# Kernel optimization log

Hardware: AMD Instinct MI355X
Metric: run time of the kernel (lower is better)

## Reference

```python
import jax, jax.numpy as jnp
import numpy as np

V, E, U, D, B, T = 32000, 256, 512, 512, 32, 64


def setup_inputs() -> dict:
    key = jax.random.key(0)
    ks = jax.random.split(key, 12)
    g = lambda k, shape: (jax.random.normal(k, shape, jnp.float32) * 0.05)
    return dict(
        x=jax.random.randint(ks[0], (B, T), 0, V),
        emb=g(ks[1], (V, E)),
        Wxf=g(ks[2], (E, 4 * U)), Whf=g(ks[3], (U, 4 * U)), bf=jnp.zeros((4 * U,), jnp.float32),
        Wxb=g(ks[4], (E, 4 * U)), Whb=g(ks[5], (U, 4 * U)), bb=jnp.zeros((4 * U,), jnp.float32),
        W1=g(ks[6], (2 * U + D, 10)), b1=jnp.zeros((10,), jnp.float32),
        W2=g(ks[7], (10, 1)), b2=jnp.zeros((1,), jnp.float32),
        Wxd=g(ks[8], (2 * U, 4 * D)), Whd=g(ks[9], (D, 4 * D)), bd=jnp.zeros((4 * D,), jnp.float32),
        Wo=g(ks[10], (D, V)), bo=jnp.zeros((V,), jnp.float32),
    )


def lstm_cell(x_t, h, c, Wx, Wh, b):
    # Keras gate order: i, f, g(cell), o
    z = x_t @ Wx + h @ Wh + b
    i, f, g, o = jnp.split(z, 4, axis=-1)
    c = jax.nn.sigmoid(f) * c + jax.nn.sigmoid(i) * jnp.tanh(g)
    h = jax.nn.sigmoid(o) * jnp.tanh(c)
    return h, c


def lstm_seq(xs, Wx, Wh, b):
    # xs: [T, B, F] -> hidden states [T, B, units]
    units = Wh.shape[0]
    h0 = jnp.zeros((xs.shape[1], units), xs.dtype)

    def step(carry, x_t):
        h, c = lstm_cell(x_t, carry[0], carry[1], Wx, Wh, b)
        return (h, c), h

    _, hs = jax.lax.scan(step, (h0, h0), xs)
    return hs


def reference(x, emb, Wxf, Whf, bf, Wxb, Whb, bb, W1, b1, W2, b2, Wxd, Whd, bd, Wo, bo):
    Bsz, Tlen = x.shape
    xe = emb[x]                              # [B, T, E]
    xs = jnp.swapaxes(xe, 0, 1)              # [T, B, E]
    hf = lstm_seq(xs, Wxf, Whf, bf)          # forward direction
    hb = lstm_seq(xs[::-1], Wxb, Whb, bb)[::-1]  # backward direction
    a = jnp.swapaxes(jnp.concatenate([hf, hb], axis=-1), 0, 1)  # [B, T, 2U]
    du = Whd.shape[0]

    def dec_step(carry, _):
        h, c = carry
        s_rep = jnp.broadcast_to(h[:, None, :], (Bsz, Tlen, du))
        cat = jnp.concatenate([a, s_rep], axis=-1)              # [B, T, 2U+D]
        e = jax.nn.relu(jnp.tanh(cat @ W1 + b1) @ W2 + b2)      # [B, T, 1]
        score = jax.nn.softmax(e, axis=1)
        ctx = jnp.sum(score * a, axis=1)                        # [B, 2U]
        h, c = lstm_cell(ctx, h, c, Wxd, Whd, bd)
        out = jax.nn.softmax(h @ Wo + bo, axis=-1)              # [B, V]
        return (h, c), out

    init = (jnp.zeros((Bsz, du), a.dtype), jnp.zeros((Bsz, du), a.dtype))
    _, outs = jax.lax.scan(dec_step, init, None, length=Tlen)
    return jnp.swapaxes(outs, 0, 1)  # [B, T, V]
```

## Files before the change

### kernel.cpp

```cpp
#include <hip/hip_runtime.h>
#include <hip/hip_bf16.h>
#include <cstdint>

typedef float f32x4 __attribute__((ext_vector_type(4)));
typedef __bf16 bf16x8 __attribute__((ext_vector_type(8)));

__device__ __forceinline__ uint32_t bf1(float x) {
  uint32_t u = __float_as_uint(x);
  return (u + 0x7fffu + ((u >> 16) & 1u)) >> 16;
}
__device__ __forceinline__ uint32_t bpack(float lo, float hi) {
  return bf1(lo) | (bf1(hi) << 16);
}
__device__ __forceinline__ float blo(uint32_t u) { return __uint_as_float(u << 16); }
__device__ __forceinline__ float bhi(uint32_t u) { return __uint_as_float(u & 0xffff0000u); }
__device__ __forceinline__ float sigm(float x) {
  return __fdividef(1.f, 1.f + exp2f(x * -1.4426950408889634f));
}
__device__ __forceinline__ float tanhf_fast(float x) {
  float e2 = exp2f(x * 2.8853900817779268f);
  return 1.f - __fdividef(2.f, e2 + 1.f);
}

__device__ __forceinline__ float dot2bf(uint32_t a, uint32_t b, float acc) {
  asm("v_dot2_f32_bf16 %0, %1, %2, %0" : "+v"(acc) : "v"(a), "v"(b));
  return acc;
}

#define GLOAD_LDS16(g, l)                                                     \
  __builtin_amdgcn_global_load_lds(                                           \
      (const __attribute__((address_space(1))) void*)(g),                     \
      (__attribute__((address_space(3))) void*)(l), 16, 0, 0)

__global__ __launch_bounds__(256) void k0_pack(
    const float* __restrict__ Whf, const float* __restrict__ Whb,
    uint32_t* __restrict__ Wencp, const float* __restrict__ Whd,
    uint32_t* __restrict__ Wdp, const float* __restrict__ W1,
    uint32_t* __restrict__ W1pbAll)
{
  int bid = blockIdx.x;
  if (bid < 4096) {
    int p = bid * 256 + threadIdx.x;
    int e = p & 3, c = (p >> 2) & 7, k4p = (p >> 5) & 63;
    int blk = (p >> 11) & 255, dir = p >> 19;
    int k2 = 4 * k4p + e;
    const float* W = dir ? Whb : Whf;
    int col = (c >> 1) * 512 + blk * 2 + (c & 1);
    Wencp[p] = bpack(W[(size_t)(2 * k2) * 2048 + col],
                     W[(size_t)(2 * k2 + 1) * 2048 + col]);
  } else if (bid < 6144) {
    int p = (bid - 4096) * 256 + threadIdx.x;
    int e = p & 3, cc = (p >> 2) & 31, q4 = (p >> 7) & 63, ug = p >> 13;
    int k2 = 4 * q4 + e;
    int col = (cc >> 3) * 512 + ug * 8 + (cc & 7);
    int k = 2 * k2;
    Wdp[p] = bpack(Whd[(size_t)k * 2048 + col], Whd[(size_t)(k + 1) * 2048 + col]);
  } else {
    int p = (bid - 6144) * 256 + threadIdx.x;
    if (p < 9216) {
      int q = p / 12, j = p % 12;
      float v0 = (j < 10) ? W1[(size_t)(2 * q) * 10 + j] : 0.f;
      float v1 = (j < 10) ? W1[(size_t)(2 * q + 1) * 10 + j] : 0.f;
      W1pbAll[p] = bpack(v0, v1);
    }
  }
}

__global__ __launch_bounds__(256) void k1_embed_gemm(
    const int* __restrict__ x, const float* __restrict__ emb,
    const float* __restrict__ Wxf, const float* __restrict__ Wxb,
    const float* __restrict__ bfv, const float* __restrict__ bbv,
    float* __restrict__ Xf, float* __restrict__ Xb)
{
  __shared__ float As[32 * 260];
  __shared__ float Bs[32 * 128];
  __shared__ int xid[32];
  const int t = threadIdx.x;
  const int ty = blockIdx.y;
  const int c0 = blockIdx.x * 128;
  if (t < 32) xid[t] = x[t * 64 + ty];
  __syncthreads();
  for (int i = 0; i < 8; ++i) {
    int f4 = t + 256 * i;
    int r = f4 >> 6, k4 = (f4 & 63) << 2;
    float4 v = *(const float4*)(emb + (size_t)xid[r] * 256 + k4);
    *(float4*)(&As[r * 260 + k4]) = v;
  }
  const int isB = (c0 >= 2048);
  const float* Wsrc = isB ? Wxb : Wxf;
  const float* bias = isB ? bbv : bfv;
  const int cbase = c0 & 2047;
  float acc[4][4] = {};
  const int rq = t >> 5;
  const int cq = t & 31;
  for (int kc = 0; kc < 8; ++kc) {
    int k0 = kc * 32;
    __syncthreads();
    for (int i = 0; i < 4; ++i) {
      int f4 = t + 256 * i;
      int k = f4 >> 5, c4 = (f4 & 31) << 2;
      *(float4*)(&Bs[k * 128 + c4]) =
          *(const float4*)(Wsrc + (size_t)(k0 + k) * 2048 + cbase + c4);
    }
    __syncthreads();
#pragma unroll
    for (int kk = 0; kk < 32; ++kk) {
      float a0 = As[(4 * rq + 0) * 260 + k0 + kk];
      float a1 = As[(4 * rq + 1) * 260 + k0 + kk];
      float a2 = As[(4 * rq + 2) * 260 + k0 + kk];
      float a3 = As[(4 * rq + 3) * 260 + k0 + kk];
      float4 b = *(const float4*)(&Bs[kk * 128 + 4 * cq]);
      acc[0][0] += a0 * b.x; acc[0][1] += a0 * b.y; acc[0][2] += a0 * b.z; acc[0][3] += a0 * b.w;
      acc[1][0] += a1 * b.x; acc[1][1] += a1 * b.y; acc[1][2] += a1 * b.z; acc[1][3] += a1 * b.w;
      acc[2][0] += a2 * b.x; acc[2][1] += a2 * b.y; acc[2][2] += a2 * b.z; acc[2][3] += a2 * b.w;
      acc[3][0] += a3 * b.x; acc[3][1] += a3 * b.y; acc[3][2] += a3 * b.z; acc[3][3] += a3 * b.w;
    }
  }
  float* Xout = isB ? Xb : Xf;
  for (int i = 0; i < 4; ++i) {
    int c = cbase + 4 * cq + i;
    float bi = bias[c];
    for (int j = 0; j < 4; ++j) {
      int b_ = 4 * rq + j;
      Xout[((size_t)ty * 2048 + c) * 32 + b_] = acc[j][i] + bi;
    }
  }
}

__global__ __launch_bounds__(256) void k2_enc_step(
    const float* __restrict__ Xf, const float* __restrict__ Xb,
    const uint32_t* __restrict__ Wencp,
    const uint32_t* __restrict__ hfi, uint32_t* __restrict__ hfo,
    const uint32_t* __restrict__ hbi, uint32_t* __restrict__ hbo,
    float* __restrict__ cf, float* __restrict__ cb,
    ushort* __restrict__ aB, int step)
{
  __shared__ uint32_t hTp[256 * 32];
  __shared__ uint32_t Wsp[2048];
  __shared__ float zx[8 * 33];
  __shared__ float zbuf[32 * 9];
  __shared__ float hl[2 * 32];
  const int t = threadIdx.x;
  const int dir = blockIdx.x >> 8;
  const int blk = blockIdx.x & 255;
  const int u0 = blk * 2;
  const float* XF = dir ? Xb : Xf;
  const uint32_t* hin = dir ? hbi : hfi;
  uint32_t* hout = dir ? hbo : hfo;
  float* cst = dir ? cb : cf;
  const int ta = dir ? (63 - step) : step;
  const uint32_t* wsrc = Wencp + ((size_t)dir * 256 + blk) * 2048;

  for (int i = 0; i < 8; ++i) {
    int b4 = (t >> 6) * 64 + 256 * i;
    GLOAD_LDS16(hin + (size_t)(t + 256 * i) * 4, hTp + (size_t)b4 * 4);
  }
  for (int i = 0; i < 2; ++i) {
    int b4 = (t >> 6) * 64 + 256 * i;
    GLOAD_LDS16(wsrc + (size_t)(t + 256 * i) * 4, Wsp + (size_t)b4 * 4);
  }
  {
    int c = t >> 5, r = t & 31;
    int col = (c >> 1) * 512 + u0 + (c & 1);
    zx[c * 33 + r] = XF[((size_t)ta * 2048 + col) * 32 + r];
  }
  __syncthreads();
  const int r = t & 31, cc = t >> 5;
  float acc = zx[cc * 33 + r];
  const uint4* hT4 = (const uint4*)hTp;
  const uint4* Ws4 = (const uint4*)Wsp;
#pragma unroll 8
  for (int k4p = 0; k4p < 64; ++k4p) {
    uint4 ua = hT4[k4p * 32 + r];
    uint4 w = Ws4[k4p * 8 + cc];
    acc = dot2bf(ua.x, w.x, acc);
    acc = dot2bf(ua.y, w.y, acc);
    acc = dot2bf(ua.z, w.z, acc);
    acc = dot2bf(ua.w, w.w, acc);
  }
  zbuf[r * 9 + cc] = acc;
  __syncthreads();
  if (t < 64) {
    int rr = t & 31, j = t >> 5;
    float zi = zbuf[rr * 9 + j];
    float zf = zbuf[rr * 9 + 2 + j];
    float zg = zbuf[rr * 9 + 4 + j];
    float zo = zbuf[rr * 9 + 6 + j];
    int u = u0 + j;
    float cold = cst[u * 32 + rr];
    float cn = sigm(zf) * cold + sigm(zi) * tanhf_fast(zg);
    float h = sigm(zo) * tanhf_fast(cn);
    cst[u * 32 + rr] = cn;
    aB[((size_t)rr * 64 + ta) * 1024 + dir * 512 + u] = (ushort)bf1(h);
    hl[j * 32 + rr] = h;
  }
  __syncthreads();
  if (t < 32) {
    hout[(blk >> 2) * 128 + t * 4 + (blk & 3)] = bpack(hl[t], hl[32 + t]);
  }
}

__global__ __launch_bounds__(256) void k5_aw1(
    const ushort* __restrict__ aB, const uint32_t* __restrict__ W1pbAll,
    const float* __restrict__ b1, float* __restrict__ aw1)
{
  __shared__ uint32_t ar[512];
  __shared__ float ps[16 * 17];
  const int t = threadIdx.x;
  const uint32_t* aBu = (const uint32_t*)aB;
  for (int m = blockIdx.x; m < 2048; m += gridDim.x) {
    __syncthreads();
    *(uint2*)(&ar[t * 2]) = *(const uint2*)(aBu + (size_t)m * 512 + t * 2);
    __syncthreads();
    int j = t & 15, part = t >> 4;
    int jj = j < 10 ? j : 0;
    float s = 0.f;
#pragma unroll 8
    for (int q = part * 32; q < part * 32 + 32; ++q)
      s = dot2bf(ar[q], W1pbAll[q * 12 + jj], s);
    ps[part * 17 + j] = s;
    __syncthreads();
    if (t < 16) {
      float sum = 0.f;
      if (t < 10) {
        for (int p = 0; p < 16; ++p) sum += ps[p * 17 + t];
        sum += b1[t];
      }
      aw1[m * 16 + t] = sum;
    }
  }
}

__global__ __launch_bounds__(256) void k_wxdT(
    const float* __restrict__ Wxd, ushort* __restrict__ WxdT)
{
  __shared__ float tile[64 * 65];
  const int t = threadIdx.x;
  const int n0 = blockIdx.x * 64, k0 = blockIdx.y * 64;
  for (int i = 0; i < 16; ++i) {
    int p = t + 256 * i;
    int kk = p >> 6, nn = p & 63;
    tile[kk * 65 + nn] = Wxd[(size_t)(k0 + kk) * 2048 + n0 + nn];
  }
  __syncthreads();
  for (int i = 0; i < 4; ++i) {
    int p = t + 256 * i;
    int nn = p >> 4, k4 = (p & 15) * 4;
    ushort4 o;
    o.x = (ushort)bf1(tile[(k4 + 0) * 65 + nn]);
    o.y = (ushort)bf1(tile[(k4 + 1) * 65 + nn]);
    o.z = (ushort)bf1(tile[(k4 + 2) * 65 + nn]);
    o.w = (ushort)bf1(tile[(k4 + 3) * 65 + nn]);
    *(ushort4*)(WxdT + (size_t)(n0 + nn) * 1024 + k0 + k4) = o;
  }
}

__global__ __launch_bounds__(256) void kA_aprime(
    const ushort* __restrict__ WxdT, const ushort* __restrict__ aB,
    uint32_t* __restrict__ ApTb)
{
  __shared__ ushort As[128 * 64];
  __shared__ ushort Bs[128 * 64];
  const int t = threadIdx.x;
  const int lane = t & 63, w = t >> 6;
  const int wr = w >> 1, wc = w & 1;
  const int m0 = blockIdx.y * 128, n0 = blockIdx.x * 128;
  const int lrow = lane >> 3, s = lane & 7;
  const int quad = lane >> 4, l15 = lane & 15;
  f32x4 acc[4][4] = {};
  for (int kc = 0; kc < 16; ++kc) {
    const int k0 = kc * 64;
    __syncthreads();
    for (int i = 0; i < 4; ++i) {
      int row = w * 32 + i * 8 + lrow;
      int k8 = s ^ (row & 7);
      GLOAD_LDS16(WxdT + (size_t)(m0 + row) * 1024 + k0 + k8 * 8,
                  As + (w * 32 + i * 8) * 64);
      GLOAD_LDS16(aB + (size_t)(n0 + row) * 1024 + k0 + k8 * 8,
                  Bs + (w * 32 + i * 8) * 64);
    }
    __syncthreads();
#pragma unroll
    for (int ks = 0; ks < 2; ++ks) {
      bf16x8 af[4], bfr[4];
      int kq = ks * 4 + quad;
#pragma unroll
      for (int mi = 0; mi < 4; ++mi) {
        int row = wr * 64 + mi * 16 + l15;
        int slot = kq ^ (row & 7);
        af[mi] = *(const bf16x8*)(As + row * 64 + slot * 8);
      }
#pragma unroll
      for (int ni = 0; ni < 4; ++ni) {
        int row = wc * 64 + ni * 16 + l15;
        int slot = kq ^ (row & 7);
        bfr[ni] = *(const bf16x8*)(Bs + row * 64 + slot * 8);
      }
#pragma unroll
      for (int mi = 0; mi < 4; ++mi)
#pragma unroll
        for (int ni = 0; ni < 4; ++ni)
          acc[mi][ni] = __builtin_amdgcn_mfma_f32_16x16x32_bf16(
              af[mi], bfr[ni], acc[mi][ni], 0, 0, 0);
    }
  }
#pragma unroll
  for (int mi = 0; mi < 4; ++mi) {
    int mbase = m0 + wr * 64 + mi * 16 + quad * 4;
#pragma unroll
    for (int reg = 0; reg < 4; ++reg) {
      int m = mbase + reg;
#pragma unroll
      for (int ni = 0; ni < 4; ++ni) {
        int n = n0 + wc * 64 + ni * 16 + l15;
        float v = acc[mi][ni][reg];
        float v2 = __shfl_xor(v, 1);
        if (!(l15 & 1))
          ApTb[(size_t)m * 1024 + (n >> 1)] = bpack(v, v2);
      }
    }
  }
}

__global__ __launch_bounds__(256) void k4_dec_step(
    const uint32_t* __restrict__ ApTb, const float* __restrict__ aw1,
    const uint32_t* __restrict__ W1pb, const float* __restrict__ W2,
    const float* __restrict__ b2, const uint32_t* __restrict__ hdp_in,
    const uint32_t* __restrict__ Wdp, const float* __restrict__ bd,
    uint32_t* __restrict__ hdp_out, float* __restrict__ cd,
    ushort* __restrict__ HsB, int step)
{
  __shared__ uint32_t W1s[256 * 12];
  __shared__ uint32_t hdT[4096];
  __shared__ uint32_t Wsp[8192];
  __shared__ float ph[32 * 8 * 12];
  __shared__ float hw1[8 * 12];
  __shared__ float esc[8 * 65];
  __shared__ uint32_t escp[8 * 33];
  __shared__ float pm[8 * 9];
  __shared__ float mrow[8], srow[8];
  __shared__ float w2s[12];
  __shared__ float zbuf[8 * 33];
  __shared__ float hl[64];
  const int t = threadIdx.x;
  const int ug = blockIdx.x >> 2;
  const int rg = blockIdx.x & 3;
  const int u0 = ug * 8, r0 = rg * 8;
  for (int i = 0; i < 3; ++i) {
    int b4 = (t >> 6) * 64 + 256 * i;
    GLOAD_LDS16(W1pb + (size_t)(t + 256 * i) * 4, W1s + (size_t)b4 * 4);
  }
  for (int i = 0; i < 4; ++i) {
    int idx4 = t + 256 * i;
    int q4 = idx4 >> 3, rl0 = idx4 & 7;
    int b4 = (t >> 6) * 64 + 256 * i;
    GLOAD_LDS16(hdp_in + (size_t)(q4 * 32 + r0 + rl0) * 4, hdT + (size_t)b4 * 4);
  }
  if (t < 12) w2s[t] = (t < 10) ? W2[t] : 0.f;
  __syncthreads();
  {
    const uint32_t* wsrc = Wdp + (size_t)ug * 8192;
    for (int i = 0; i < 8; ++i) {
      int b4 = (t >> 6) * 64 + 256 * i;
      GLOAD_LDS16(wsrc + (size_t)(t + 256 * i) * 4, Wsp + (size_t)b4 * 4);
    }
  }
  {
    const int rl = t & 7, kp = t >> 3;
    const uint4* hd4 = (const uint4*)hdT;
    float acc[10] = {};
    for (int q4 = kp * 2; q4 < kp * 2 + 2; ++q4) {
      uint4 u4 = hd4[q4 * 8 + rl];
      const uint32_t* w0 = &W1s[(4 * q4) * 12];
      const uint32_t* w1 = &W1s[(4 * q4 + 1) * 12];
      const uint32_t* w2p = &W1s[(4 * q4 + 2) * 12];
      const uint32_t* w3 = &W1s[(4 * q4 + 3) * 12];
#pragma unroll
      for (int j = 0; j < 10; ++j) {
        acc[j] = dot2bf(u4.x, w0[j], acc[j]);
        acc[j] = dot2bf(u4.y, w1[j], acc[j]);
        acc[j] = dot2bf(u4.z, w2p[j], acc[j]);
        acc[j] = dot2bf(u4.w, w3[j], acc[j]);
      }
    }
#pragma unroll
    for (int j = 0; j < 10; ++j) ph[(kp * 8 + rl) * 12 + j] = acc[j];
  }
  __syncthreads();
  if (t < 96) {
    int rl = t / 12, j = t % 12;
    float s = 0.f;
#pragma unroll
    for (int p = 0; p < 32; ++p) s += ph[(p * 8 + rl) * 12 + j];
    hw1[rl * 12 + j] = s;
  }
  __syncthreads();
  const float b2v = b2[0];
  for (int p = 0; p < 2; ++p) {
    int idx = t + 256 * p;
    int rl = idx >> 6, tt = idx & 63;
    size_t m = (size_t)(r0 + rl) * 64 + tt;
    const float4* aw = (const float4*)(aw1 + m * 16);
    float4 q0 = aw[0], q1 = aw[1], q2 = aw[2];
    const float* hw = &hw1[rl * 12];
    float e = b2v;
    e += tanhf_fast(q0.x + hw[0]) * w2s[0];
    e += tanhf_fast(q0.y + hw[1]) * w2s[1];
    e += tanhf_fast(q0.z + hw[2]) * w2s[2];
    e += tanhf_fast(q0.w + hw[3]) * w2s[3];
    e += tanhf_fast(q1.x + hw[4]) * w2s[4];
    e += tanhf_fast(q1.y + hw[5]) * w2s[5];
    e += tanhf_fast(q1.z + hw[6]) * w2s[6];
    e += tanhf_fast(q1.w + hw[7]) * w2s[7];
    e += tanhf_fast(q2.x + hw[8]) * w2s[8];
    e += tanhf_fast(q2.y + hw[9]) * w2s[9];
    esc[rl * 65 + tt] = fmaxf(e, 0.f);
  }
  __syncthreads();
  if (t < 64) {
    int rl = t >> 3, part = t & 7;
    float m = -1e30f;
    for (int i = 0; i < 8; ++i) m = fmaxf(m, esc[rl * 65 + part * 8 + i]);
    pm[rl * 9 + part] = m;
  }
  __syncthreads();
  if (t < 8) {
    float m = pm[t * 9];
    for (int p = 1; p < 8; ++p) m = fmaxf(m, pm[t * 9 + p]);
    mrow[t] = m;
  }
  __syncthreads();
  if (t < 64) {
    int rl = t >> 3, part = t & 7;
    float m = mrow[rl];
    float s = 0.f;
    for (int i = 0; i < 8; ++i) s += __expf(esc[rl * 65 + part * 8 + i] - m);
    pm[rl * 9 + part] = s;
  }
  __syncthreads();
  if (t < 8) {
    float s = 0.f;
    for (int p = 0; p < 8; ++p) s += pm[t * 9 + p];
    srow[t] = __fdividef(1.f, s);
  }
  __syncthreads();
  {
    int rl = t >> 5, q = t & 31;
    float m = mrow[rl], s = srow[rl];
    float v0 = __expf(esc[rl * 65 + 2 * q] - m) * s;
    float v1 = __expf(esc[rl * 65 + 2 * q + 1] - m) * s;
    escp[rl * 33 + q] = bpack(v0, v1);
  }
  __syncthreads();
  const int ccB = t >> 3, rl = t & 7;
  const int colg = (ccB >> 3) * 512 + u0 + (ccB & 7);
  float acc = 0.f;
  {
    const uint4* hd4 = (const uint4*)hdT;
    const uint4* wd4 = (const uint4*)Wsp;
#pragma unroll 8
    for (int q4 = 0; q4 < 64; ++q4) {
      uint4 ua = hd4[q4 * 8 + rl];
      uint4 ub = wd4[q4 * 32 + ccB];
      acc = dot2bf(ua.x, ub.x, acc);
      acc = dot2bf(ua.y, ub.y, acc);
      acc = dot2bf(ua.z, ub.z, acc);
      acc = dot2bf(ua.w, ub.w, acc);
    }
  }
  {
    const uint32_t* ap = ApTb + (size_t)colg * 1024 + (r0 + rl) * 32;
    const uint32_t* ep = &escp[rl * 33];
#pragma unroll
    for (int i8 = 0; i8 < 8; ++i8) {
      uint4 v = *(const uint4*)(ap + i8 * 4);
      acc = dot2bf(v.x, ep[4 * i8 + 0], acc);
      acc = dot2bf(v.y, ep[4 * i8 + 1], acc);
      acc = dot2bf(v.z, ep[4 * i8 + 2], acc);
      acc = dot2bf(v.w, ep[4 * i8 + 3], acc);
    }
  }
  zbuf[rl * 33 + ccB] = acc + bd[colg];
  __syncthreads();
  if (t < 64) {
    int j = t >> 3, rr = t & 7;
    int u = u0 + j, rgl = r0 + rr;
    float zi = zbuf[rr * 33 + j];
    float zf = zbuf[rr * 33 + 8 + j];
    float zg = zbuf[rr * 33 + 16 + j];
    float zo = zbuf[rr * 33 + 24 + j];
    float cold = cd[u * 32 + rgl];
    float cn = sigm(zf) * cold + sigm(zi) * tanhf_fast(zg);
    float h = sigm(zo) * tanhf_fast(cn);
    cd[u * 32 + rgl] = cn;
    HsB[(size_t)(step * 32 + rgl) * 512 + u] = (ushort)bf1(h);
    hl[j * 8 + rr] = h;
  }
  __syncthreads();
  if (t < 32) {
    int p = t >> 3, rr = t & 7;
    hdp_out[ug * 128 + (r0 + rr) * 4 + p] =
        bpack(hl[(2 * p) * 8 + rr], hl[(2 * p + 1) * 8 + rr]);
  }
}

__global__ __launch_bounds__(256) void k_woT(
    const float* __restrict__ Wo, ushort* __restrict__ WoT)
{
  __shared__ float tile[64 * 65];
  const int t = threadIdx.x;
  const int n0 = blockIdx.x * 64, k0 = blockIdx.y * 64;
  for (int i = 0; i < 16; ++i) {
    int p = t + 256 * i;
    int kk = p >> 6, nn = p & 63;
    tile[kk * 65 + nn] = Wo[(size_t)(k0 + kk) * 32000 + n0 + nn];
  }
  __syncthreads();
  for (int i = 0; i < 4; ++i) {
    int p = t + 256 * i;
    int nn = p >> 4, k4 = (p & 15) * 4;
    ushort4 o;
    o.x = (ushort)bf1(tile[(k4 + 0) * 65 + nn]);
    o.y = (ushort)bf1(tile[(k4 + 1) * 65 + nn]);
    o.z = (ushort)bf1(tile[(k4 + 2) * 65 + nn]);
    o.w = (ushort)bf1(tile[(k4 + 3) * 65 + nn]);
    *(ushort4*)(WoT + (size_t)(n0 + nn) * 512 + k0 + k4) = o;
  }
}

__global__ __launch_bounds__(256) void k6_logits_mfma(
    const ushort* __restrict__ HsB, const ushort* __restrict__ WoT,
    const float* __restrict__ bo, float* __restrict__ out,
    float2* __restrict__ pstats, int moff)
{
  __shared__ ushort As[128 * 64];
  __shared__ ushort Bs[128 * 64];
  const int t = threadIdx.x;
  const int lane = t & 63, w = t >> 6;
  const int wr = w >> 1, wc = w & 1;
  const int m0 = (blockIdx.y + moff) * 128, n0 = blockIdx.x * 128;
  const int lrow = lane >> 3, s = lane & 7;
  const int quad = lane >> 4, l15 = lane & 15;
  f32x4 acc[4][4] = {};
  for (int kc = 0; kc < 8; ++kc) {
    const int k0 = kc * 64;
    __syncthreads();
    for (int i = 0; i < 4; ++i) {
      int row = w * 32 + i * 8 + lrow;
      int k8 = s ^ (row & 7);
      GLOAD_LDS16(HsB + (size_t)(m0 + row) * 512 + k0 + k8 * 8,
                  As + (w * 32 + i * 8) * 64);
      GLOAD_LDS16(WoT + (size_t)(n0 + row) * 512 + k0 + k8 * 8,
                  Bs + (w * 32 + i * 8) * 64);
    }
    __syncthreads();
#pragma unroll
    for (int ks = 0; ks < 2; ++ks) {
      bf16x8 af[4], bfr[4];
      int kq = ks * 4 + quad;
#pragma unroll
      for (int mi = 0; mi < 4; ++mi) {
        int row = wr * 64 + mi * 16 + l15;
        int slot = kq ^ (row & 7);
        af[mi] = *(const bf16x8*)(As + row * 64 + slot * 8);
      }
#pragma unroll
      for (int ni = 0; ni < 4; ++ni) {
        int row = wc * 64 + ni * 16 + l15;
        int slot = kq ^ (row & 7);
        bfr[ni] = *(const bf16x8*)(Bs + row * 64 + slot * 8);
      }
#pragma unroll
      for (int mi = 0; mi < 4; ++mi)
#pragma unroll
        for (int ni = 0; ni < 4; ++ni)
          acc[mi][ni] = __builtin_amdgcn_mfma_f32_16x16x32_bf16(
              af[mi], bfr[ni], acc[mi][ni], 0, 0, 0);
    }
  }
  __syncthreads();
  float* pmx = (float*)As;
  float* psm = (float*)Bs;
#pragma unroll
  for (int mi = 0; mi < 4; ++mi) {
    int mbase = m0 + wr * 64 + mi * 16 + quad * 4;
#pragma unroll
    for (int reg = 0; reg < 4; ++reg) {
      int m = mbase + reg;
      int rowl = (m - m0);
      size_t rowbase = ((size_t)(m & 31) * 64 + (m >> 5)) * 32000;
      float vs[4];
      float mx = -1e30f;
#pragma unroll
      for (int ni = 0; ni < 4; ++ni) {
        int n = n0 + wc * 64 + ni * 16 + l15;
        float v = acc[mi][ni][reg] + bo[n];
        out[rowbase + n] = v;
        vs[ni] = v;
        mx = fmaxf(mx, v);
      }
      float sl = __expf(vs[0] - mx) + __expf(vs[1] - mx) +
                 __expf(vs[2] - mx) + __expf(vs[3] - mx);
      pmx[rowl * 32 + wc * 16 + l15] = mx;
      psm[rowl * 32 + wc * 16 + l15] = sl;
    }
  }
  __syncthreads();
  if (t < 128) {
    float m = pmx[t * 32], sacc = psm[t * 32];
    for (int i = 1; i < 32; ++i) {
      float m2 = pmx[t * 32 + i], s2 = psm[t * 32 + i];
      float mn = fmaxf(m, m2);
      sacc = sacc * __expf(m - mn) + s2 * __expf(m2 - mn);
      m = mn;
    }
    int mg = m0 + t;
    int outrow = (mg & 31) * 64 + (mg >> 5);
    pstats[(size_t)outrow * 256 + blockIdx.x] = make_float2(m, sacc);
  }
}

__global__ __launch_bounds__(256) void k7_softmax(
    float* __restrict__ out, const float2* __restrict__ pstats, int half)
{
  __shared__ float mred[256], sred[256];
  const int t = threadIdx.x;
  const int mg = half * 1024 + blockIdx.x;
  const int row = (mg & 31) * 64 + (mg >> 5);
  float m = -1e30f, s = 0.f;
  if (t < 250) {
    float2 p = pstats[(size_t)row * 256 + t];
    m = p.x;
    s = p.y;
  }
  mred[t] = m;
  sred[t] = s;
  __syncthreads();
  for (int st = 128; st > 0; st >>= 1) {
    if (t < st) {
      float m1 = mred[t], m2 = mred[t + st];
      float mn = fmaxf(m1, m2);
      sred[t] = sred[t] * __expf(m1 - mn) + sred[t + st] * __expf(m2 - mn);
      mred[t] = mn;
    }
    __syncthreads();
  }
  m = mred[0];
  const float inv = 1.f / sred[0];
  float* p = out + (size_t)row * 32000;
  for (int i = t; i < 8000; i += 256) {
    float4 v = *(const float4*)(p + i * 4);
    v.x = __expf(v.x - m) * inv;
    v.y = __expf(v.y - m) * inv;
    v.z = __expf(v.z - m) * inv;
    v.w = __expf(v.w - m) * inv;
    *(float4*)(p + i * 4) = v;
  }
}

extern "C" void kernel_launch(void* const* d_in, const int* in_sizes, int n_in,
                              void* d_out, int out_size, void* d_ws, size_t ws_size,
                              hipStream_t stream)
{
  const int* x = (const int*)d_in[0];
  const float* emb = (const float*)d_in[1];
  const float* Wxf = (const float*)d_in[2];
  const float* Whf = (const float*)d_in[3];
  const float* bfv = (const float*)d_in[4];
  const float* Wxb = (const float*)d_in[5];
  const float* Whb = (const float*)d_in[6];
  const float* bbv = (const float*)d_in[7];
  const float* W1 = (const float*)d_in[8];
  const float* b1 = (const float*)d_in[9];
  const float* W2 = (const float*)d_in[10];
  const float* b2 = (const float*)d_in[11];
  const float* Wxd = (const float*)d_in[12];
  const float* Whd = (const float*)d_in[13];
  const float* bd = (const float*)d_in[14];
  const float* Wo = (const float*)d_in[15];
  const float* bo = (const float*)d_in[16];

  float* ws = (float*)d_ws;
  float* c_f = ws + 0;
  float* c_b = ws + 16384;
  float* c_d = ws + 32768;
  uint32_t* hfp0 = (uint32_t*)(ws + 49152);
  uint32_t* hfp1 = hfp0 + 8192;
  uint32_t* hbp0 = (uint32_t*)(ws + 65536);
  uint32_t* hbp1 = hbp0 + 8192;
  uint32_t* hdp0 = (uint32_t*)(ws + 81920);
  uint32_t* hdp1 = hdp0 + 8192;
  uint32_t* W1pbAll = (uint32_t*)(ws + 98304);
  uint32_t* Wencp = (uint32_t*)(ws + 114688);
  uint32_t* Wdp = (uint32_t*)(ws + 1163264);
  ushort* aB = (ushort*)(ws + 1687552);
  float* aw1 = ws + 2742272;
  float* Xf = ws + 2775040;
  float* Xb = Xf + 4194304;
  ushort* HsB = (ushort*)(ws + 13260800);
  uint32_t* ApTb = (uint32_t*)Xf;
  ushort* WxdT = (ushort*)Xb;
  ushort* WoT = (ushort*)Xf;
  float2* pstats = (float2*)Wencp;

  hipMemsetAsync(ws, 0, 98304 * sizeof(float), stream);

  k0_pack<<<6180, 256, 0, stream>>>(Whf, Whb, Wencp, Whd, Wdp, W1, W1pbAll);

  k1_embed_gemm<<<dim3(32, 64), 256, 0, stream>>>(x, emb, Wxf, Wxb, bfv, bbv, Xf, Xb);

  for (int s = 0; s < 64; ++s) {
    const uint32_t* hfi = (s & 1) ? hfp1 : hfp0;
    uint32_t* hfo = (s & 1) ? hfp0 : hfp1;
    const uint32_t* hbi = (s & 1) ? hbp1 : hbp0;
    uint32_t* hbo = (s & 1) ? hbp0 : hbp1;
    k2_enc_step<<<512, 256, 0, stream>>>(Xf, Xb, Wencp, hfi, hfo, hbi, hbo,
                                         c_f, c_b, aB, s);
  }

  k5_aw1<<<256, 256, 0, stream>>>(aB, W1pbAll, b1, aw1);
  k_wxdT<<<dim3(32, 16), 256, 0, stream>>>(Wxd, WxdT);
  kA_aprime<<<dim3(16, 16), 256, 0, stream>>>(WxdT, aB, ApTb);

  for (int s = 0; s < 64; ++s) {
    const uint32_t* hdi = (s & 1) ? hdp1 : hdp0;
    uint32_t* hdo = (s & 1) ? hdp0 : hdp1;
    k4_dec_step<<<256, 256, 0, stream>>>(ApTb, aw1, W1pbAll + 6144, W2, b2,
                                         hdi, Wdp, bd, hdo, c_d, HsB, s);
  }

  k_woT<<<dim3(500, 8), 256, 0, stream>>>(Wo, WoT);
  k6_logits_mfma<<<dim3(250, 8), 256, 0, stream>>>(HsB, WoT, bo,
                                                   (float*)d_out, pstats, 0);
  k7_softmax<<<1024, 256, 0, stream>>>((float*)d_out, pstats, 0);
  k6_logits_mfma<<<dim3(250, 8), 256, 0, stream>>>(HsB, WoT, bo,
                                                   (float*)d_out, pstats, 8);
  k7_softmax<<<1024, 256, 0, stream>>>((float*)d_out, pstats, 1);
}
```

Baseline: 1.634 ms.

## Split decoder step over 512 blocks of 4 batch rows with split-K gate dot

The decoder step kernel now assigns 4 batch rows per block instead of 8, doubling the grid to 512 blocks. The gate dot product is split across two halves of K so that all 256 threads do useful work, and a new shared buffer reduces the two partial sums. The goal is to fill more CUs and shorten each block's serial latency on the latency-bound recurrent step. In exchange, each block still loads the full 32 KB recurrent weight slice, so total weight traffic doubles, and the extra reduction adds a barrier.

```diff
diff --git a/kernel.cpp b/kernel.cpp
--- a/kernel.cpp
+++ b/kernel.cpp
@@ -331,29 +331,29 @@
     ushort* __restrict__ HsB, int step)
 {
   __shared__ uint32_t W1s[256 * 12];
-  __shared__ uint32_t hdT[4096];
+  __shared__ uint32_t hdT[1024];
   __shared__ uint32_t Wsp[8192];
-  __shared__ float ph[32 * 8 * 12];
-  __shared__ float hw1[8 * 12];
-  __shared__ float esc[8 * 65];
-  __shared__ uint32_t escp[8 * 33];
-  __shared__ float pm[8 * 9];
-  __shared__ float mrow[8], srow[8];
+  __shared__ float ph[64 * 4 * 12];
+  __shared__ float hw1[4 * 12];
+  __shared__ float esc[4 * 65];
+  __shared__ uint32_t escp[4 * 33];
+  __shared__ float pm[4 * 9];
+  __shared__ float mrow[4], srow[4];
   __shared__ float w2s[12];
-  __shared__ float zbuf[8 * 33];
-  __shared__ float hl[64];
-  const int t = threadIdx.x;
-  const int ug = blockIdx.x >> 2;
-  const int rg = blockIdx.x & 3;
-  const int u0 = ug * 8, r0 = rg * 8;
+  __shared__ float zp[2][128];
+  __shared__ float zbuf[4 * 33];
+  __shared__ float hl[32];
+  const int t = threadIdx.x;
+  const int ug = blockIdx.x >> 3;
+  const int rg = blockIdx.x & 7;
+  const int u0 = ug * 8, r0 = rg * 4;
   for (int i = 0; i < 3; ++i) {
     int b4 = (t >> 6) * 64 + 256 * i;
     GLOAD_LDS16(W1pb + (size_t)(t + 256 * i) * 4, W1s + (size_t)b4 * 4);
   }
-  for (int i = 0; i < 4; ++i) {
-    int idx4 = t + 256 * i;
-    int q4 = idx4 >> 3, rl0 = idx4 & 7;
-    int b4 = (t >> 6) * 64 + 256 * i;
+  {
+    int q4 = t >> 2, rl0 = t & 3;
+    int b4 = (t >> 6) * 64;
     GLOAD_LDS16(hdp_in + (size_t)(q4 * 32 + r0 + rl0) * 4, hdT + (size_t)b4 * 4);
   }
   if (t < 12) w2s[t] = (t < 10) ? W2[t] : 0.f;
@@ -366,15 +366,15 @@
     }
   }
   {
-    const int rl = t & 7, kp = t >> 3;
+    const int rl = t & 3, kp = t >> 2;
     const uint4* hd4 = (const uint4*)hdT;
     float acc[10] = {};
-    for (int q4 = kp * 2; q4 < kp * 2 + 2; ++q4) {
-      uint4 u4 = hd4[q4 * 8 + rl];
-      const uint32_t* w0 = &W1s[(4 * q4) * 12];
-      const uint32_t* w1 = &W1s[(4 * q4 + 1) * 12];
-      const uint32_t* w2p = &W1s[(4 * q4 + 2) * 12];
-      const uint32_t* w3 = &W1s[(4 * q4 + 3) * 12];
+    {
+      uint4 u4 = hd4[kp * 4 + rl];
+      const uint32_t* w0 = &W1s[(4 * kp) * 12];
+      const uint32_t* w1 = &W1s[(4 * kp + 1) * 12];
+      const uint32_t* w2p = &W1s[(4 * kp + 2) * 12];
+      const uint32_t* w3 = &W1s[(4 * kp + 3) * 12];
 #pragma unroll
       for (int j = 0; j < 10; ++j) {
         acc[j] = dot2bf(u4.x, w0[j], acc[j]);
@@ -384,21 +384,20 @@
       }
     }
 #pragma unroll
-    for (int j = 0; j < 10; ++j) ph[(kp * 8 + rl) * 12 + j] = acc[j];
-  }
-  __syncthreads();
-  if (t < 96) {
-    int rl = t / 12, j = t % 12;
+    for (int j = 0; j < 10; ++j) ph[(kp * 4 + rl) * 12 + j] = acc[j];
+  }
+  __syncthreads();
+  if (t < 40) {
+    int rl = t / 10, j = t % 10;
     float s = 0.f;
 #pragma unroll
-    for (int p = 0; p < 32; ++p) s += ph[(p * 8 + rl) * 12 + j];
+    for (int p = 0; p < 64; ++p) s += ph[(p * 4 + rl) * 12 + j];
     hw1[rl * 12 + j] = s;
   }
   __syncthreads();
   const float b2v = b2[0];
-  for (int p = 0; p < 2; ++p) {
-    int idx = t + 256 * p;
-    int rl = idx >> 6, tt = idx & 63;
+  {
+    int rl = t >> 6, tt = t & 63;
     size_t m = (size_t)(r0 + rl) * 64 + tt;
     const float4* aw = (const float4*)(aw1 + m * 16);
     float4 q0 = aw[0], q1 = aw[1], q2 = aw[2];
@@ -417,20 +416,20 @@
     esc[rl * 65 + tt] = fmaxf(e, 0.f);
   }
   __syncthreads();
-  if (t < 64) {
+  if (t < 32) {
     int rl = t >> 3, part = t & 7;
     float m = -1e30f;
     for (int i = 0; i < 8; ++i) m = fmaxf(m, esc[rl * 65 + part * 8 + i]);
     pm[rl * 9 + part] = m;
   }
   __syncthreads();
-  if (t < 8) {
+  if (t < 4) {
     float m = pm[t * 9];
     for (int p = 1; p < 8; ++p) m = fmaxf(m, pm[t * 9 + p]);
     mrow[t] = m;
   }
   __syncthreads();
-  if (t < 64) {
+  if (t < 32) {
     int rl = t >> 3, part = t & 7;
     float m = mrow[rl];
     float s = 0.f;
@@ -438,13 +437,13 @@
     pm[rl * 9 + part] = s;
   }
   __syncthreads();
-  if (t < 8) {
+  if (t < 4) {
     float s = 0.f;
     for (int p = 0; p < 8; ++p) s += pm[t * 9 + p];
     srow[t] = __fdividef(1.f, s);
   }
   __syncthreads();
-  {
+  if (t < 128) {
     int rl = t >> 5, q = t & 31;
     float m = mrow[rl], s = srow[rl];
     float v0 = __expf(esc[rl * 65 + 2 * q] - m) * s;
@@ -452,38 +451,48 @@
     escp[rl * 33 + q] = bpack(v0, v1);
   }
   __syncthreads();
-  const int ccB = t >> 3, rl = t & 7;
-  const int colg = (ccB >> 3) * 512 + u0 + (ccB & 7);
-  float acc = 0.f;
   {
-    const uint4* hd4 = (const uint4*)hdT;
-    const uint4* wd4 = (const uint4*)Wsp;
+    const int out = t & 127;
+    const int ccB = out >> 2, rl = out & 3;
+    const int kh = t >> 7;
+    const int colg = (ccB >> 3) * 512 + u0 + (ccB & 7);
+    float acc = 0.f;
+    {
+      const uint4* hd4 = (const uint4*)hdT;
+      const uint4* wd4 = (const uint4*)Wsp;
 #pragma unroll 8
-    for (int q4 = 0; q4 < 64; ++q4) {
-      uint4 ua = hd4[q4 * 8 + rl];
-      uint4 ub = wd4[q4 * 32 + ccB];
-      acc = dot2bf(ua.x, ub.x, acc);
-      acc = dot2bf(ua.y, ub.y, acc);
-      acc = dot2bf(ua.z, ub.z, acc);
-      acc = dot2bf(ua.w, ub.w, acc);
-    }
-  }
-  {
-    const uint32_t* ap = ApTb + (size_t)colg * 1024 + (r0 + rl) * 32;
-    const uint32_t* ep = &escp[rl * 33];
-#pragma unroll
-    for (int i8 = 0; i8 < 8; ++i8) {
-      uint4 v = *(const uint4*)(ap + i8 * 4);
-      acc = dot2bf(v.x, ep[4 * i8 + 0], acc);
-      acc = dot2bf(v.y, ep[4 * i8 + 1], acc);
-      acc = dot2bf(v.z, ep[4 * i8 + 2], acc);
-      acc = dot2bf(v.w, ep[4 * i8 + 3], acc);
-    }
-  }
-  zbuf[rl * 33 + ccB] = acc + bd[colg];
-  __syncthreads();
-  if (t < 64) {
-    int j = t >> 3, rr = t & 7;
+      for (int q4 = kh * 32; q4 < kh * 32 + 32; ++q4) {
+        uint4 ua = hd4[q4 * 4 + rl];
+        uint4 ub = wd4[q4 * 32 + ccB];
+        acc = dot2bf(ua.x, ub.x, acc);
+        acc = dot2bf(ua.y, ub.y, acc);
+        acc = dot2bf(ua.z, ub.z, acc);
+        acc = dot2bf(ua.w, ub.w, acc);
+      }
+    }
+    {
+      const uint32_t* ap = ApTb + (size_t)colg * 1024 + (r0 + rl) * 32;
+      const uint32_t* ep = &escp[rl * 33];
+#pragma unroll
+      for (int i8 = kh * 4; i8 < kh * 4 + 4; ++i8) {
+        uint4 v = *(const uint4*)(ap + i8 * 4);
+        acc = dot2bf(v.x, ep[4 * i8 + 0], acc);
+        acc = dot2bf(v.y, ep[4 * i8 + 1], acc);
+        acc = dot2bf(v.z, ep[4 * i8 + 2], acc);
+        acc = dot2bf(v.w, ep[4 * i8 + 3], acc);
+      }
+    }
+    zp[kh][out] = acc;
+  }
+  __syncthreads();
+  if (t < 128) {
+    int ccB = t >> 2, rl = t & 3;
+    int colg = (ccB >> 3) * 512 + u0 + (ccB & 7);
+    zbuf[rl * 33 + ccB] = zp[0][t] + zp[1][t] + bd[colg];
+  }
+  __syncthreads();
+  if (t < 32) {
+    int j = t >> 2, rr = t & 3;
     int u = u0 + j, rgl = r0 + rr;
     float zi = zbuf[rr * 33 + j];
     float zf = zbuf[rr * 33 + 8 + j];
@@ -494,13 +503,13 @@
     float h = sigm(zo) * tanhf_fast(cn);
     cd[u * 32 + rgl] = cn;
     HsB[(size_t)(step * 32 + rgl) * 512 + u] = (ushort)bf1(h);
-    hl[j * 8 + rr] = h;
-  }
-  __syncthreads();
-  if (t < 32) {
-    int p = t >> 3, rr = t & 7;
+    hl[j * 4 + rr] = h;
+  }
+  __syncthreads();
+  if (t < 16) {
+    int p = t >> 2, rr = t & 3;
     hdp_out[ug * 128 + (r0 + rr) * 4 + p] =
-        bpack(hl[(2 * p) * 8 + rr], hl[(2 * p + 1) * 8 + rr]);
+        bpack(hl[(2 * p) * 4 + rr], hl[(2 * p + 1) * 4 + rr]);
   }
 }
 
@@ -725,7 +734,7 @@
   for (int s = 0; s < 64; ++s) {
     const uint32_t* hdi = (s & 1) ? hdp1 : hdp0;
     uint32_t* hdo = (s & 1) ? hdp0 : hdp1;
-    k4_dec_step<<<256, 256, 0, stream>>>(ApTb, aw1, W1pbAll + 6144, W2, b2,
+    k4_dec_step<<<512, 256, 0, stream>>>(ApTb, aw1, W1pbAll + 6144, W2, b2,
                                          hdi, Wdp, bd, hdo, c_d, HsB, s);
   }
 
```

Result: no change. 1.612 ms (-1.4%).
